# Performance work log

Hardware: AMD Instinct MI355X
Metric: run time of the kernel (lower is better)

The kernel has to match this reference:

```python
import jax, jax.numpy as jnp
import numpy as np

B, DIM, NX, NY = 4, 64, 256, 256
HEADS, DIM_HEAD, LATENT, DIM_OUT, KM = 4, 32, 128, 64, 2
DH = DIM_HEAD * KM  # LowRankKernel head dim (also RoPE dim) = 64
EPS = 1e-5
MIN_FREQ = 1.0 / 64.0  # RotaryEmbedding default in FactFormer/LNS repo


def _gelu(x):
    return jax.nn.gelu(x, approximate=False)  # torch nn.GELU default (erf)


def _conv1x1(u, w):
    # u: [b,c,h,w], w: [out,c]  (1x1 conv == channel matmul)
    return jnp.einsum('bchw,oc->bohw', u, w)


def _pooling_reducer(x, win, ln_g, ln_b, w1, w2, b2):
    # x: [b, n_keep, n_pool, c] -> Linear, mean-pool over n_pool, LN+FFN
    h = jnp.einsum('bnmc,hc->bnmh', x, win).mean(axis=2)  # [b, n, hid]
    m = h.mean(axis=-1, keepdims=True)
    v = h.var(axis=-1, keepdims=True)
    h = (h - m) / jnp.sqrt(v + EPS) * ln_g + ln_b
    return _gelu(h @ w1.T) @ w2.T + b2  # [b, n, latent]


def _rope_freqs(n):
    pos = jnp.linspace(0.0, 1.0, n) / MIN_FREQ  # scale/min_freq = 64
    inv = 1.0 / (10000.0 ** (jnp.arange(0, DH, 2, dtype=jnp.float32) / DH))
    f = pos[:, None] * inv[None, :]            # [n, DH//2]
    return jnp.concatenate([f, f], axis=-1)    # [n, DH]


def _apply_rope(x, f):
    # rotate_half = cat(-x2, x1) on half-split (FactFormer convention)
    d = x.shape[-1] // 2
    rot = jnp.concatenate([-x[..., d:], x[..., :d]], axis=-1)
    return x * jnp.cos(f) + rot * jnp.sin(f)


def _low_rank_kernel(x, wqk):
    # x: [b, n, latent] -> K: [b, heads, n, n]; scaling=1, dropout=Identity, qk_norm=False
    b, n, _ = x.shape
    qk = x @ wqk.T
    q, k = jnp.split(qk, 2, axis=-1)
    q = q.reshape(b, n, HEADS, DH).transpose(0, 2, 1, 3)
    k = k.reshape(b, n, HEADS, DH).transpose(0, 2, 1, 3)
    f = _rope_freqs(n)
    q = _apply_rope(q, f)
    k = _apply_rope(k, f)
    return jnp.einsum('bhid,bhjd->bhij', q, k)


def _forward(u, gn_w, gn_b, w_in_proj, w_to_in,
             px_win, px_ln_g, px_ln_b, px_w1, px_w2, px_b2,
             py_win, py_ln_g, py_ln_b, py_w1, py_w2, py_b2,
             kx_wqk, ky_wqk, out_w1, out_w2):
    # GroupNorm(1, dim): normalize over (C,H,W) per sample, affine
    m = u.mean(axis=(1, 2, 3), keepdims=True)
    v = u.var(axis=(1, 2, 3), keepdims=True)
    un = (u - m) / jnp.sqrt(v + EPS) * gn_w[None, :, None, None] + gn_b[None, :, None, None]
    u_phi = _conv1x1(un, w_in_proj)  # [b, heads*dim_head, nx, ny]
    ui = _conv1x1(un, w_to_in)       # [b, dim, nx, ny]
    # to_x: pool over ny -> tokens along nx; to_y: pool over nx -> tokens along ny
    ux = _pooling_reducer(ui.transpose(0, 2, 3, 1), px_win, px_ln_g, px_ln_b, px_w1, px_w2, px_b2)  # [b, nx, latent]
    uy = _pooling_reducer(ui.transpose(0, 3, 2, 1), py_win, py_ln_g, py_ln_b, py_w1, py_w2, py_b2)  # [b, ny, latent]
    kx = _low_rank_kernel(ux, kx_wqk)  # [b, h, nx, nx]
    ky = _low_rank_kernel(uy, ky_wqk)  # [b, h, ny, ny]
    b, hc, nx, ny = u_phi.shape
    up = u_phi.reshape(b, HEADS, hc // HEADS, nx, ny)
    up = jnp.einsum('bhij,bhcjm->bhcim', kx, up)
    up = jnp.einsum('bhlm,bhcim->bhcil', ky, up)
    up = up.reshape(b, hc, nx, ny)
    # InstanceNorm2d (no affine, no running stats)
    m2 = up.mean(axis=(2, 3), keepdims=True)
    v2 = up.var(axis=(2, 3), keepdims=True)
    upn = (up - m2) / jnp.sqrt(v2 + EPS)
    out = _conv1x1(_gelu(_conv1x1(upn, out_w1)), out_w2)
    return out + u


def setup_inputs() -> dict:
    key = jax.random.key(0)
    ks = jax.random.split(key, 16)
    def w(k, shape, s=0.02):
        return (jax.random.normal(k, shape) * s).astype(jnp.float32)
    return {
        'u': jax.random.normal(ks[0], (B, DIM, NX, NY), dtype=jnp.float32),
        'gn_w': jnp.ones((DIM,), jnp.float32), 'gn_b': jnp.zeros((DIM,), jnp.float32),
        'w_in_proj': w(ks[1], (HEADS * DIM_HEAD, DIM)),
        'w_to_in': w(ks[2], (DIM, DIM)),
        'px_win': w(ks[3], (DIM, DIM)),
        'px_ln_g': jnp.ones((DIM,), jnp.float32), 'px_ln_b': jnp.zeros((DIM,), jnp.float32),
        'px_w1': w(ks[4], (2 * DIM, DIM)), 'px_w2': w(ks[5], (LATENT, 2 * DIM)),
        'px_b2': jnp.zeros((LATENT,), jnp.float32),
        'py_win': w(ks[6], (DIM, DIM)),
        'py_ln_g': jnp.ones((DIM,), jnp.float32), 'py_ln_b': jnp.zeros((DIM,), jnp.float32),
        'py_w1': w(ks[7], (2 * DIM, DIM)), 'py_w2': w(ks[8], (LATENT, 2 * DIM)),
        'py_b2': jnp.zeros((LATENT,), jnp.float32),
        'kx_wqk': w(ks[9], (2 * HEADS * DH, LATENT)),
        'ky_wqk': w(ks[10], (2 * HEADS * DH, LATENT)),
        'out_w1': w(ks[11], (DIM_OUT, HEADS * DIM_HEAD)),
        'out_w2': w(ks[12], (DIM_OUT, DIM_OUT)),
    }


def reference(u, gn_w, gn_b, w_in_proj, w_to_in,
              px_win, px_ln_g, px_ln_b, px_w1, px_w2, px_b2,
              py_win, py_ln_g, py_ln_b, py_w1, py_w2, py_b2,
              kx_wqk, ky_wqk, out_w1, out_w2):
    return _forward(u, gn_w, gn_b, w_in_proj, w_to_in,
                    px_win, px_ln_g, px_ln_b, px_w1, px_w2, px_b2,
                    py_win, py_ln_g, py_ln_b, py_w1, py_w2, py_b2,
                    kx_wqk, ky_wqk, out_w1, out_w2)
```

## Files before the change

### kernel.cpp

```cpp
#include <hip/hip_runtime.h>
#include <math.h>

typedef unsigned short ushort_t;
typedef unsigned int uint_t;
typedef __attribute__((ext_vector_type(8))) short s8v;
typedef __attribute__((ext_vector_type(4))) float f4;

#define NPIX 65536
#define EPS_ 1e-5f

__device__ __forceinline__ float bf2f(ushort_t u){ return __uint_as_float(((uint_t)u)<<16); }
__device__ __forceinline__ ushort_t f2bf(float f){
  uint_t u = __float_as_uint(f);
  uint_t r = (u + 0x7fffu + ((u>>16)&1u)) >> 16;
  return (ushort_t)r;
}
__device__ __forceinline__ float bflo(uint_t p){ return __uint_as_float(p<<16); }
__device__ __forceinline__ float bfhi(uint_t p){ return __uint_as_float(p & 0xffff0000u); }
__device__ __forceinline__ uint_t packbf(float a, float b){ return (uint_t)f2bf(a) | ((uint_t)f2bf(b)<<16); }

__device__ __forceinline__ f4 MFMA(s8v a, s8v b, f4 c){
  return __builtin_amdgcn_mfma_f32_16x16x32_bf16(a, b, c, 0, 0, 0);
}

__device__ __forceinline__ float wave_sum(float v){
  #pragma unroll
  for(int m=32;m>=1;m>>=1) v += __shfl_xor(v, m, 64);
  return v;
}

__global__ __launch_bounds__(256) void k1_stats(const float* __restrict__ u,
    float* __restrict__ part, float* __restrict__ pc, float* __restrict__ poolx){
  int blk = blockIdx.x; int b = blk>>8; int c = (blk>>2)&63; int iq = blk&3;
  int t = threadIdx.x; int lane = t&63; int w = t>>6;
  const float* up = u + ((size_t)(b*64+c))*NPIX + iq*64*256;
  __shared__ float red[8];
  float cs=0.f, ss=0.f;
  for(int r=0;r<64;r++){
    float v = up[r*256 + t];
    cs += v; ss += v*v;
  }
  pc[((b*64+c)*4 + iq)*256 + t] = cs;
  float a1 = wave_sum(cs), a2 = wave_sum(ss);
  if(lane==0){ red[w]=a1; red[4+w]=a2; }
  __syncthreads();
  if(t==0){
    part[((b*64+c)*4+iq)*2]   = red[0]+red[1]+red[2]+red[3];
    part[((b*64+c)*4+iq)*2+1] = red[4]+red[5]+red[6]+red[7];
  }
  int r = t>>2, ck = t&3;
  const float* rp = up + r*256 + ck*64;
  float s=0.f;
  #pragma unroll 4
  for(int j=0;j<16;j++){
    float4 v4 = *(const float4*)(rp + j*4);
    s += v4.x + v4.y + v4.z + v4.w;
  }
  s += __shfl_xor(s, 1, 64);
  s += __shfl_xor(s, 2, 64);
  if(ck==0) poolx[(b*256 + iq*64 + r)*64 + c] = s * (1.f/256.f);
}

__global__ void k2_fin(const float* __restrict__ part, float* __restrict__ gnmv){
  int t = threadIdx.x; int b = t>>6; int i = t&63;
  float S1=0.f, S2=0.f;
  #pragma unroll
  for(int q=0;q<4;q++){
    S1 += part[((b*64+i)*4+q)*2];
    S2 += part[((b*64+i)*4+q)*2+1];
  }
  S1 = wave_sum(S1); S2 = wave_sum(S2);
  if(i==0){
    const float inv = 1.f/4194304.f;
    float m = S1*inv; float v = S2*inv - m*m;
    gnmv[b*2] = m; gnmv[b*2+1] = rsqrtf(v + EPS_);
  }
}

__global__ __launch_bounds__(256) void k2b_pool(const float* __restrict__ pc,
    float* __restrict__ pooly){
  int blk = blockIdx.x; int b = blk>>6; int c = blk&63;
  int t = threadIdx.x;
  const float* p = pc + ((size_t)(b*64+c))*4*256 + t;
  float s = p[0] + p[256] + p[512] + p[768];
  pooly[(b*256+t)*64 + c] = s * (1.f/256.f);
}

__global__ __launch_bounds__(256) void k8a_fold(const float* __restrict__ gnmv,
    const float* __restrict__ gnw, const float* __restrict__ gnb,
    const float* __restrict__ w_in_proj, const float* __restrict__ out_w2,
    ushort_t* __restrict__ wpb, float* __restrict__ c0g, ushort_t* __restrict__ w2b){
  int b = blockIdx.x; int t = threadIdx.x;
  __shared__ float scs[64], shs[64];
  if(t<64){
    float mean = gnmv[b*2], rstd = gnmv[b*2+1];
    float sc = rstd*gnw[t];
    scs[t] = sc; shs[t] = gnb[t] - mean*sc;
  }
  __syncthreads();
  int oc = t>>1, h = t&1;
  float c0 = 0.f;
  for(int k=0;k<32;k++){
    int ch = h*32 + k;
    float wv = w_in_proj[oc*64 + ch];
    wpb[((size_t)b*128 + oc)*64 + ch] = f2bf(wv*scs[ch]);
    c0 += wv*shs[ch];
  }
  c0 += __shfl_xor(c0, 1, 64);
  if(h==0) c0g[b*128 + oc] = c0;
  if(b==0){
    for(int e=t;e<4096;e+=256) w2b[e] = f2bf(out_w2[e]);
  }
}

__global__ void k8b_fold(const float* __restrict__ istat,
    const float* __restrict__ out_w1, ushort_t* __restrict__ W1b,
    float* __restrict__ bias1){
  int b = blockIdx.x; int t = threadIdx.x;
  __shared__ float ms[128], rss[128];
  ms[t] = istat[(b*128+t)*2];       rss[t] = istat[(b*128+t)*2+1];
  ms[64+t] = istat[(b*128+64+t)*2]; rss[64+t] = istat[(b*128+64+t)*2+1];
  __syncthreads();
  float bias = 0.f;
  for(int ch=0;ch<128;ch++){
    float wv = out_w1[t*128 + ch];
    float wr = wv*rss[ch];
    W1b[((size_t)b*64 + t)*128 + ch] = f2bf(wr);
    bias += wr*ms[ch];
  }
  bias1[b*64 + t] = bias;
}

__global__ __launch_bounds__(128) void k3_reduce(
    const float* __restrict__ poolx, const float* __restrict__ pooly,
    const float* __restrict__ gnmv,
    const float* __restrict__ gnw, const float* __restrict__ gnb,
    const float* __restrict__ w_to_in,
    const float* __restrict__ xwin, const float* __restrict__ xlg, const float* __restrict__ xlb,
    const float* __restrict__ xw1, const float* __restrict__ xw2, const float* __restrict__ xb2,
    const float* __restrict__ ywin, const float* __restrict__ ylg, const float* __restrict__ ylb,
    const float* __restrict__ yw1, const float* __restrict__ yw2, const float* __restrict__ yb2,
    float* __restrict__ ux, float* __restrict__ uy){
  int id = blockIdx.x;
  int side = id >> 10; int r = id & 1023; int b = r>>8; int i = r&255;
  const float* pool = side ? pooly : poolx;
  const float* win = side ? ywin : xwin;
  const float* lg  = side ? ylg  : xlg;
  const float* lb  = side ? ylb  : xlb;
  const float* w1  = side ? yw1  : xw1;
  const float* w2  = side ? yw2  : xw2;
  const float* b2  = side ? yb2  : xb2;
  float* outp = side ? uy : ux;
  int t = threadIdx.x;
  __shared__ float pn[64], t1[64], hh[64], f1[128];
  float mean = gnmv[b*2], rstd = gnmv[b*2+1];
  if(t<64){
    float pv = pool[(b*256+i)*64 + t];
    pn[t] = (pv - mean)*rstd*gnw[t] + gnb[t];
  }
  __syncthreads();
  if(t<64){
    float acc=0.f; const float* wr = w_to_in + t*64;
    #pragma unroll 8
    for(int c=0;c<64;c++) acc += pn[c]*wr[c];
    t1[t]=acc;
  }
  __syncthreads();
  if(t<64){
    float acc=0.f; const float* wr = win + t*64;
    #pragma unroll 8
    for(int c=0;c<64;c++) acc += t1[c]*wr[c];
    hh[t]=acc;
  }
  __syncthreads();
  if(t<64){
    float v = hh[t];
    float s = wave_sum(v);
    float ss = wave_sum(v*v);
    float m2 = s*(1.f/64.f);
    float var = ss*(1.f/64.f) - m2*m2;
    float rs2 = rsqrtf(var + EPS_);
    hh[t] = (v - m2)*rs2*lg[t] + lb[t];
  }
  __syncthreads();
  {
    float acc=0.f; const float* wr = w1 + t*64;
    #pragma unroll 8
    for(int c=0;c<64;c++) acc += hh[c]*wr[c];
    f1[t] = 0.5f*acc*(1.f + erff(acc*0.70710678118654752f));
  }
  __syncthreads();
  {
    float acc=0.f; const float* wr = w2 + t*128;
    #pragma unroll 8
    for(int j=0;j<128;j++) acc += f1[j]*wr[j];
    outp[(b*256+i)*128 + t] = acc + b2[t];
  }
}

__global__ __launch_bounds__(256) void k4_gemm(
    const float* __restrict__ ux, const float* __restrict__ uy,
    const float* __restrict__ wqkx, const float* __restrict__ wqky,
    ushort_t* __restrict__ qxb, ushort_t* __restrict__ kxTb,
    ushort_t* __restrict__ qyb, ushort_t* __restrict__ kyTb){
  int blk = blockIdx.x;
  int nt = blk&3; int mt = (blk>>2)&1; int b = (blk>>3)&3; int side = blk>>5;
  const float* x  = (side? uy:ux) + (size_t)(b*256 + mt*128)*128;
  const float* wq = (side? wqky:wqkx) + (size_t)nt*128*128;
  ushort_t* qb  = side? qyb : qxb;
  ushort_t* kTb = side? kyTb : kxTb;

  __shared__ __align__(16) ushort_t sA[128*136];
  __shared__ __align__(16) ushort_t sB[128*136];

  int t = threadIdx.x; int lane = t&63; int w = t>>6; int lr = lane&15; int lg = lane>>4;
  for(int e=t;e<4096;e+=256){
    int row = e>>5, c4 = (e&31)*4;
    float4 v = *(const float4*)(x + row*128 + c4);
    uint2 pk; pk.x = packbf(v.x,v.y); pk.y = packbf(v.z,v.w);
    *(uint2*)&sA[row*136 + c4] = pk;
    float4 wv = *(const float4*)(wq + row*128 + c4);
    uint2 wk; wk.x = packbf(wv.x,wv.y); wk.y = packbf(wv.z,wv.w);
    *(uint2*)&sB[row*136 + c4] = wk;
  }
  __syncthreads();
  const f4 fz = {0.f,0.f,0.f,0.f};
  f4 acc[2][8];
  #pragma unroll
  for(int it=0;it<2;it++)
    #pragma unroll
    for(int n2=0;n2<8;n2++) acc[it][n2]=fz;
  #pragma unroll
  for(int kc=0;kc<4;kc++){
    s8v bf[8];
    #pragma unroll
    for(int n2=0;n2<8;n2++)
      bf[n2] = *(const s8v*)&sB[(n2*16+lr)*136 + kc*32 + lg*8];
    #pragma unroll
    for(int it=0;it<2;it++){
      s8v a = *(const s8v*)&sA[(w*32+it*16+lr)*136 + kc*32 + lg*8];
      #pragma unroll
      for(int n2=0;n2<8;n2++)
        acc[it][n2] = MFMA(a, bf[n2], acc[it][n2]);
    }
  }
  if(nt < 2){
    #pragma unroll
    for(int it=0;it<2;it++){
      #pragma unroll
      for(int n2=0;n2<8;n2++){
        int o = nt*128 + n2*16 + lr;
        int h = o>>6, dd = o&63, t32 = dd&31;
        float invf = expf(-(float)t32*(9.210340371976184f/32.f));
        size_t base = (size_t)(b*4+h)*16384;
        #pragma unroll
        for(int r=0;r<4;r++){
          int i = mt*128 + w*32 + it*16 + lg*4 + r;
          float f = (64.f/255.f)*(float)i*invf;
          float sn, cs; __sincosf(f, &sn, &cs);
          float pair = acc[it][n2^2][r];
          float rot = ((n2&2)==0)? -pair : pair;
          float v = acc[it][n2][r]*cs + rot*sn;
          qb[base + (size_t)i*64 + dd] = f2bf(v);
        }
      }
    }
  } else {
    __syncthreads();
    #pragma unroll
    for(int it=0;it<2;it++){
      #pragma unroll
      for(int n2=0;n2<8;n2++){
        int ol = n2*16 + lr;
        int o = nt*128 + ol;
        int t32 = o&31;
        float invf = expf(-(float)t32*(9.210340371976184f/32.f));
        #pragma unroll
        for(int r=0;r<4;r++){
          int il = w*32 + it*16 + lg*4 + r;
          int i = mt*128 + il;
          float f = (64.f/255.f)*(float)i*invf;
          float sn, cs; __sincosf(f, &sn, &cs);
          float pair = acc[it][n2^2][r];
          float rot = ((n2&2)==0)? -pair : pair;
          float v = acc[it][n2][r]*cs + rot*sn;
          sA[ol*136 + il] = f2bf(v);
        }
      }
    }
    __syncthreads();
    {
      int row = t>>1, half = t&1;
      int h = (nt-2)*2 + (row>>6), dd = row&63;
      ushort_t* dst = kTb + (size_t)(b*4+h)*16384 + (size_t)dd*256 + mt*128 + half*64;
      const ushort_t* src = &sA[row*136 + half*64];
      #pragma unroll
      for(int j=0;j<8;j++)
        *(uint4*)(dst + j*8) = *(const uint4*)(src + j*8);
    }
  }
}

__global__ __launch_bounds__(256) void k5s_sums(const ushort_t* __restrict__ kxTb,
    const ushort_t* __restrict__ kyTb, float* __restrict__ ksum){
  int bh = blockIdx.x; int t = threadIdx.x;
  int row = t>>2, g = t&3;
  const ushort_t* kx = kxTb + (size_t)bh*16384 + row*256 + g*64;
  float s = 0.f;
  #pragma unroll
  for(int j=0;j<8;j++){
    uint4 v = *(const uint4*)(kx + j*8);
    s += bflo(v.x)+bfhi(v.x)+bflo(v.y)+bfhi(v.y)+bflo(v.z)+bfhi(v.z)+bflo(v.w)+bfhi(v.w);
  }
  s += __shfl_xor(s,1,64); s += __shfl_xor(s,2,64);
  if(g==0) ksum[bh*128 + row] = s;
  const ushort_t* ky = kyTb + (size_t)bh*16384 + row*256 + g*64;
  float s2 = 0.f;
  #pragma unroll
  for(int j=0;j<8;j++){
    uint4 v = *(const uint4*)(ky + j*8);
    s2 += bflo(v.x)+bfhi(v.x)+bflo(v.y)+bfhi(v.y)+bflo(v.z)+bfhi(v.z)+bflo(v.w)+bfhi(v.w);
  }
  s2 += __shfl_xor(s2,1,64); s2 += __shfl_xor(s2,2,64);
  if(g==0) ksum[bh*128 + 64 + row] = s2;
}

__global__ __launch_bounds__(512) void k7a_core(
    const float* __restrict__ u,
    const ushort_t* __restrict__ kxTb, const ushort_t* __restrict__ kyTb,
    ushort_t* __restrict__ Cb){
  int blk = blockIdx.x; int b = blk>>6;
  const float* up = u + (size_t)blk*NPIX;
  __shared__ __align__(16) ushort_t su[2][64*264];
  __shared__ __align__(16) ushort_t sT1[4][64*68];
  int t = threadIdx.x; int w = t>>6; int lane = t&63; int lr = lane&15; int lg = lane>>4;
  int h = w>>1, sub = w&1;
  const ushort_t* KyT = kyTb + (size_t)(b*4+h)*16384;
  const ushort_t* KxT = kxTb + (size_t)(b*4+h)*16384;
  const f4 fz = {0.f,0.f,0.f,0.f};
  f4 cacc[2][4];
  #pragma unroll
  for(int it=0;it<2;it++)
    #pragma unroll
    for(int et=0;et<4;et++) cacc[it][et]=fz;

  auto stageld = [&](int jc, int buf){
    #pragma unroll
    for(int k=0;k<8;k++){
      int flat = k*512 + t;
      int row = flat>>6, col4 = flat&63;
      float4 v = *(const float4*)(up + (size_t)(jc*64+row)*256 + col4*4);
      uint2 pk; pk.x = packbf(v.x,v.y); pk.y = packbf(v.z,v.w);
      *(uint2*)&su[buf][row*264 + col4*4] = pk;
    }
  };
  stageld(0, 0);
  __syncthreads();
  for(int jc=0;jc<4;jc++){
    int cur = jc&1;
    f4 acc[2][4];
    #pragma unroll
    for(int jt=0;jt<2;jt++)
      #pragma unroll
      for(int et=0;et<4;et++) acc[jt][et]=fz;
    #pragma unroll
    for(int km=0;km<8;km++){
      s8v a0 = *(const s8v*)&su[cur][(sub*32+lr)*264 + km*32 + lg*8];
      s8v a1 = *(const s8v*)&su[cur][(sub*32+16+lr)*264 + km*32 + lg*8];
      #pragma unroll
      for(int et=0;et<4;et++){
        s8v bv = *(const s8v*)(KyT + (et*16+lr)*256 + km*32 + lg*8);
        acc[0][et] = MFMA(a0,bv,acc[0][et]);
        acc[1][et] = MFMA(a1,bv,acc[1][et]);
      }
    }
    #pragma unroll
    for(int jt=0;jt<2;jt++)
      #pragma unroll
      for(int et=0;et<4;et++){
        f4 v = acc[jt][et];
        uint2 pk; pk.x=packbf(v.x,v.y); pk.y=packbf(v.z,v.w);
        *(uint2*)&sT1[h][(et*16+lr)*68 + sub*32 + jt*16 + lg*4] = pk;
      }
    __syncthreads();
    if(jc<3) stageld(jc+1, cur^1);
    #pragma unroll
    for(int kj=0;kj<2;kj++){
      s8v a0 = *(const s8v*)(KxT + (size_t)(sub*32+lr)*256 + jc*64 + kj*32 + lg*8);
      s8v a1 = *(const s8v*)(KxT + (size_t)(sub*32+16+lr)*256 + jc*64 + kj*32 + lg*8);
      #pragma unroll
      for(int et=0;et<4;et++){
        s8v bv = *(const s8v*)&sT1[h][(et*16+lr)*68 + kj*32 + lg*8];
        cacc[0][et] = MFMA(a0,bv,cacc[0][et]);
        cacc[1][et] = MFMA(a1,bv,cacc[1][et]);
      }
    }
    __syncthreads();
  }
  ushort_t* cbase = Cb + ((size_t)blk*4 + h)*4096;
  #pragma unroll
  for(int it=0;it<2;it++)
    #pragma unroll
    for(int et=0;et<4;et++){
      f4 v = cacc[it][et];
      uint2 pk; pk.x=packbf(v.x,v.y); pk.y=packbf(v.z,v.w);
      *(uint2*)&cbase[(et*16+lr)*64 + sub*32 + it*16 + lg*4] = pk;
    }
}

__global__ __launch_bounds__(256) void k7b_heavy(
    const ushort_t* __restrict__ Cb, const ushort_t* __restrict__ wpb,
    const float* __restrict__ c0g, const float* __restrict__ ksum,
    const ushort_t* __restrict__ qxb, const ushort_t* __restrict__ qyb,
    ushort_t* __restrict__ up2, float* __restrict__ istat){
  int blk = blockIdx.x;
  int c = blk & 31; int h = (blk>>5)&3; int b = blk>>7;
  int bh = b*4 + h; int ch = h*32 + c;
  const ushort_t* Qx  = qxb + (size_t)bh*16384;
  const ushort_t* Qy  = qyb + (size_t)bh*16384;
  ushort_t* out_c = up2 + (size_t)(b*128 + ch)*NPIX;

  __shared__ __align__(16) ushort_t sCT[64*72];
  __shared__ __align__(16) ushort_t sP[256*72];
  __shared__ float sW[64], sKx[64], sKy[64];
  __shared__ float sRed[8];

  int t = threadIdx.x; int w = t>>6; int lane = t&63; int lr = lane&15; int lg = lane>>4;
  if(t<64){
    sW[t]  = bf2f(wpb[((size_t)b*128 + ch)*64 + t]);
    sKx[t] = ksum[bh*128 + t];
    sKy[t] = ksum[bh*128 + 64 + t];
  }
  __syncthreads();
  {
    int e = t>>2, d0 = (t&3)*16;
    float c0 = c0g[b*128 + ch];
    float kyv = sKy[e];
    float acc[16];
    #pragma unroll
    for(int k=0;k<16;k++) acc[k] = c0*kyv*sKx[d0+k];
    const ushort_t* cbp = Cb + ((size_t)(b*64)*4 + h)*4096 + e*64 + d0;
    for(int ic=0;ic<64;ic++){
      float wv = sW[ic];
      uint4 v0 = *(const uint4*)(cbp);
      uint4 v1 = *(const uint4*)(cbp + 8);
      cbp += 16384;
      uint_t vs[8] = {v0.x,v0.y,v0.z,v0.w,v1.x,v1.y,v1.z,v1.w};
      #pragma unroll
      for(int k=0;k<8;k++){
        acc[2*k]   += wv*bflo(vs[k]);
        acc[2*k+1] += wv*bfhi(vs[k]);
      }
    }
    #pragma unroll
    for(int k=0;k<8;k++)
      *(uint_t*)&sCT[e*72 + d0 + 2*k] = packbf(acc[2*k], acc[2*k+1]);
  }
  __syncthreads();
  const f4 fz = {0.f,0.f,0.f,0.f};
  {
    s8v aF[4][2];
    #pragma unroll
    for(int me=0;me<4;me++)
      #pragma unroll
      for(int kd=0;kd<2;kd++)
        aF[me][kd] = *(const s8v*)&sCT[(me*16+lr)*72 + kd*32 + lg*8];
    #pragma unroll
    for(int it=0;it<4;it++){
      s8v b0 = *(const s8v*)(Qx + (w*64+it*16+lr)*64 + lg*8);
      s8v b1 = *(const s8v*)(Qx + (w*64+it*16+lr)*64 + 32 + lg*8);
      #pragma unroll
      for(int me=0;me<4;me++){
        f4 pv = MFMA(aF[me][0], b0, fz);
        pv = MFMA(aF[me][1], b1, pv);
        uint2 pk; pk.x=packbf(pv.x,pv.y); pk.y=packbf(pv.z,pv.w);
        *(uint2*)&sP[(w*64+it*16+lr)*72 + me*16 + lg*4] = pk;
      }
    }
  }
  __syncthreads();
  float lsum=0.f, lssq=0.f;
  {
    s8v aP[4][2];
    #pragma unroll
    for(int it=0;it<4;it++)
      #pragma unroll
      for(int ke=0;ke<2;ke++)
        aP[it][ke] = *(const s8v*)&sP[(w*64+it*16+lr)*72 + ke*32 + lg*8];
    for(int lt=0;lt<4;lt++){
      s8v bq[4][2];
      #pragma unroll
      for(int nt=0;nt<4;nt++)
        #pragma unroll
        for(int ke=0;ke<2;ke++)
          bq[nt][ke] = *(const s8v*)(Qy + (lt*64+nt*16+lr)*64 + ke*32 + lg*8);
      #pragma unroll
      for(int it=0;it<4;it++){
        #pragma unroll
        for(int nt=0;nt<4;nt++){
          f4 o = MFMA(aP[it][0], bq[nt][0], fz);
          o = MFMA(aP[it][1], bq[nt][1], o);
          #pragma unroll
          for(int r=0;r<4;r++){
            float val = o[r];
            lsum += val; lssq += val*val;
            out_c[(size_t)(w*64 + it*16 + lg*4 + r)*256 + lt*64 + nt*16 + lr] = f2bf(val);
          }
        }
      }
    }
  }
  float a1 = wave_sum(lsum), a2 = wave_sum(lssq);
  if(lane==0){ sRed[w]=a1; sRed[4+w]=a2; }
  __syncthreads();
  if(t==0){
    float S = sRed[0]+sRed[1]+sRed[2]+sRed[3];
    float SS = sRed[4]+sRed[5]+sRed[6]+sRed[7];
    float m = S*(1.f/65536.f);
    float var = SS*(1.f/65536.f) - m*m;
    istat[(b*128+ch)*2] = m;
    istat[(b*128+ch)*2+1] = rsqrtf(var + EPS_);
  }
}

__global__ __launch_bounds__(256) void kf_out(
    const ushort_t* __restrict__ up2, const ushort_t* __restrict__ W1b,
    const float* __restrict__ bias1, const ushort_t* __restrict__ w2b,
    const float* __restrict__ u, float* __restrict__ out){
  int blk = blockIdx.x;
  int b = blk>>9; int pix0 = (blk&511)<<7;
  __shared__ __align__(16) unsigned char smraw[128*132*2];
  ushort_t* sX = (ushort_t*)smraw;
  ushort_t* sG = (ushort_t*)smraw;
  float* sO = (float*)smraw;
  int t = threadIdx.x; int lane = t&63; int w = t>>6; int lr = lane&15; int lg = lane>>4;
  float4 ur[8];
  {
    int oc = t>>5; int px = (t&31)*4;
    #pragma unroll
    for(int it=0;it<8;it++){
      int o = it*8 + oc;
      ur[it] = *(const float4*)(u + ((size_t)(b*64+o))*NPIX + pix0 + px);
    }
  }
  {
    int ch = t>>4; int px = (t&15)*8;
    #pragma unroll
    for(int it=0; it<8; it++){
      int c = it*16 + ch;
      uint4 v = *(const uint4*)(up2 + ((size_t)(b*128+c))*NPIX + pix0 + px);
      uint2 lo; lo.x = v.x; lo.y = v.y;
      uint2 hi; hi.x = v.z; hi.y = v.w;
      *(uint2*)&sX[c*132 + px] = lo;
      *(uint2*)&sX[c*132 + px + 4] = hi;
    }
  }
  __syncthreads();
  const ushort_t* w1p = W1b + (size_t)b*64*128;
  f4 g[2][4];
  #pragma unroll
  for(int it=0;it<2;it++)
    #pragma unroll
    for(int nt=0;nt<4;nt++){
      float bv = -bias1[b*64 + nt*16 + lr];
      f4 ci = {bv,bv,bv,bv};
      g[it][nt] = ci;
    }
  #pragma unroll
  for(int kc=0;kc<4;kc++){
    s8v bf[4];
    #pragma unroll
    for(int nt=0;nt<4;nt++)
      bf[nt] = *(const s8v*)(w1p + (nt*16+lr)*128 + kc*32 + lg*8);
    #pragma unroll
    for(int it=0;it<2;it++){
      int pix = w*32 + it*16 + lr;
      s8v a;
      #pragma unroll
      for(int j=0;j<8;j++) a[j] = (short)sX[(kc*32+lg*8+j)*132 + pix];
      #pragma unroll
      for(int nt=0;nt<4;nt++)
        g[it][nt] = MFMA(a, bf[nt], g[it][nt]);
    }
  }
  #pragma unroll
  for(int it=0;it<2;it++)
    #pragma unroll
    for(int nt=0;nt<4;nt++){
      f4 v = g[it][nt];
      #pragma unroll
      for(int r=0;r<4;r++){
        float x = v[r];
        v[r] = 0.5f*x*(1.f + erff(x*0.70710678118654752f));
      }
      g[it][nt] = v;
    }
  __syncthreads();
  #pragma unroll
  for(int it=0;it<2;it++)
    #pragma unroll
    for(int nt=0;nt<4;nt++){
      f4 v = g[it][nt];
      uint2 pk; pk.x = packbf(v.x,v.y); pk.y = packbf(v.z,v.w);
      *(uint2*)&sG[(nt*16+lr)*132 + w*32 + it*16 + lg*4] = pk;
    }
  __syncthreads();
  f4 o2[2][4];
  const f4 fz = {0.f,0.f,0.f,0.f};
  #pragma unroll
  for(int it=0;it<2;it++)
    #pragma unroll
    for(int nt=0;nt<4;nt++) o2[it][nt]=fz;
  #pragma unroll
  for(int kc=0;kc<2;kc++){
    s8v bf[4];
    #pragma unroll
    for(int nt=0;nt<4;nt++)
      bf[nt] = *(const s8v*)(w2b + (nt*16+lr)*64 + kc*32 + lg*8);
    #pragma unroll
    for(int it=0;it<2;it++){
      int pix = w*32 + it*16 + lr;
      s8v a;
      #pragma unroll
      for(int j=0;j<8;j++) a[j] = (short)sG[(kc*32+lg*8+j)*132 + pix];
      #pragma unroll
      for(int nt=0;nt<4;nt++)
        o2[it][nt] = MFMA(a, bf[nt], o2[it][nt]);
    }
  }
  __syncthreads();
  #pragma unroll
  for(int it=0;it<2;it++)
    #pragma unroll
    for(int nt=0;nt<4;nt++)
      *(f4*)&sO[(nt*16+lr)*132 + w*32 + it*16 + lg*4] = o2[it][nt];
  __syncthreads();
  {
    int oc = t>>5; int px = (t&31)*4;
    #pragma unroll
    for(int it=0;it<8;it++){
      int o = it*8 + oc;
      float4 ov = *(const float4*)&sO[o*132 + px];
      float4 rv;
      rv.x = ov.x+ur[it].x; rv.y = ov.y+ur[it].y; rv.z = ov.z+ur[it].z; rv.w = ov.w+ur[it].w;
      *(float4*)(out + ((size_t)(b*64+o))*NPIX + pix0 + px) = rv;
    }
  }
}

extern "C" void kernel_launch(void* const* d_in, const int* in_sizes, int n_in,
                              void* d_out, int out_size, void* d_ws, size_t ws_size,
                              hipStream_t stream) {
  (void)in_sizes; (void)n_in; (void)out_size; (void)ws_size;
  const float* u        = (const float*)d_in[0];
  const float* gnw      = (const float*)d_in[1];
  const float* gnb      = (const float*)d_in[2];
  const float* w_in_proj= (const float*)d_in[3];
  const float* w_to_in  = (const float*)d_in[4];
  const float* px_win   = (const float*)d_in[5];
  const float* px_ln_g  = (const float*)d_in[6];
  const float* px_ln_b  = (const float*)d_in[7];
  const float* px_w1    = (const float*)d_in[8];
  const float* px_w2    = (const float*)d_in[9];
  const float* px_b2    = (const float*)d_in[10];
  const float* py_win   = (const float*)d_in[11];
  const float* py_ln_g  = (const float*)d_in[12];
  const float* py_ln_b  = (const float*)d_in[13];
  const float* py_w1    = (const float*)d_in[14];
  const float* py_w2    = (const float*)d_in[15];
  const float* py_b2    = (const float*)d_in[16];
  const float* kx_wqk   = (const float*)d_in[17];
  const float* ky_wqk   = (const float*)d_in[18];
  const float* out_w1   = (const float*)d_in[19];
  const float* out_w2   = (const float*)d_in[20];
  float* out = (float*)d_out;

  float* fw = (float*)d_ws;
  float* part  = fw + 0;
  float* gnmv  = fw + 2048;
  float* pc    = fw + 4096;
  float* poolx = fw + 266240;
  float* pooly = fw + 331776;
  float* ux    = fw + 397312;
  float* uy    = fw + 528384;
  float* istat = fw + 659456;
  float* c0g   = fw + 660480;
  float* bias1 = fw + 660992;
  ushort_t* wpb = (ushort_t*)(fw + 661504);
  ushort_t* W1b = (ushort_t*)(fw + 677888);
  ushort_t* w2b = (ushort_t*)(fw + 694272);
  float* ksum   = fw + 696320;
  ushort_t* qxb  = (ushort_t*)(fw + 4096);
  ushort_t* kxTb = (ushort_t*)(fw + 135168);
  ushort_t* qyb  = (ushort_t*)(fw + 698368);
  ushort_t* kyTb = (ushort_t*)(fw + 829440);
  ushort_t* up2  = (ushort_t*)(fw + 960512);
  ushort_t* Cb = (ushort_t*)d_out;

  k1_stats<<<dim3(1024), dim3(256), 0, stream>>>(u, part, pc, poolx);
  k2_fin<<<dim3(1), dim3(256), 0, stream>>>(part, gnmv);
  k2b_pool<<<dim3(256), dim3(256), 0, stream>>>(pc, pooly);
  k8a_fold<<<dim3(4), dim3(256), 0, stream>>>(gnmv, gnw, gnb, w_in_proj, out_w2, wpb, c0g, w2b);
  k3_reduce<<<dim3(2048), dim3(128), 0, stream>>>(poolx, pooly, gnmv, gnw, gnb, w_to_in,
      px_win, px_ln_g, px_ln_b, px_w1, px_w2, px_b2,
      py_win, py_ln_g, py_ln_b, py_w1, py_w2, py_b2, ux, uy);
  k4_gemm<<<dim3(64), dim3(256), 0, stream>>>(ux, uy, kx_wqk, ky_wqk, qxb, kxTb, qyb, kyTb);
  k5s_sums<<<dim3(16), dim3(256), 0, stream>>>(kxTb, kyTb, ksum);
  k7a_core<<<dim3(256), dim3(512), 0, stream>>>(u, kxTb, kyTb, Cb);
  k7b_heavy<<<dim3(512), dim3(256), 0, stream>>>(Cb, wpb, c0g, ksum, qxb, qyb, up2, istat);
  k8b_fold<<<dim3(4), dim3(64), 0, stream>>>(istat, out_w1, W1b, bias1);
  kf_out<<<dim3(2048), dim3(256), 0, stream>>>(up2, W1b, bias1, w2b, u, out);
}
```

Baseline: 222.0 us.

## Split channel-mix out of heavy kernel and halve output kernel tile

Moves the per-channel mixing of the core matrices (weighted sum over 64 input channels) out of k7b_heavy into a separate k7m_mix kernel. The new kernel stages each core tile once in shared memory and reuses it across 32 output channels, where before every heavy block re-read all 64 input-channel cores from global memory. The mixed result goes to a scratch area inside the output buffer. Separately, kf_out now handles 64 pixels per block instead of 128, doubling the grid and cutting shared memory and register use. This costs an extra kernel launch and a global round trip for the mixed matrices.

```diff
diff --git a/kernel.cpp b/kernel.cpp
--- a/kernel.cpp
+++ b/kernel.cpp
@@ -408,9 +408,67 @@
     }
 }
 
-__global__ __launch_bounds__(256) void k7b_heavy(
+__global__ __launch_bounds__(256) void k7m_mix(
     const ushort_t* __restrict__ Cb, const ushort_t* __restrict__ wpb,
     const float* __restrict__ c0g, const float* __restrict__ ksum,
+    ushort_t* __restrict__ cT){
+  int blk = blockIdx.x; int bh = blk>>4; int et = blk&15;
+  int b = bh>>2, h = bh&3;
+  __shared__ __align__(16) ushort_t sC[64*264];
+  __shared__ float sWf[32*64];
+  __shared__ float sKx[64], sKy4[4];
+  int t = threadIdx.x;
+  #pragma unroll
+  for(int k=0;k<8;k++){
+    int flat = k*256 + t;
+    int ic = flat>>5, q = flat&31;
+    uint4 v = *(const uint4*)(Cb + ((size_t)(b*64+ic)*4 + h)*4096 + et*256 + q*8);
+    *(uint4*)&sC[ic*264 + q*8] = v;
+  }
+  for(int e=t;e<2048;e+=256){
+    int ch = e>>6, ic = e&63;
+    sWf[e] = bf2f(wpb[((size_t)b*128 + h*32 + ch)*64 + ic]);
+  }
+  if(t<64) sKx[t] = ksum[bh*128 + t];
+  if(t<4)  sKy4[t] = ksum[bh*128 + 64 + et*4 + t];
+  __syncthreads();
+  int chg = t>>5, edq = t&31, ed0 = edq*8;
+  float c0v[4];
+  #pragma unroll
+  for(int cc=0;cc<4;cc++) c0v[cc] = c0g[b*128 + h*32 + chg*4 + cc];
+  float acc[4][8];
+  #pragma unroll
+  for(int j=0;j<8;j++){
+    int ed = ed0 + j;
+    float r1 = sKy4[ed>>6]*sKx[ed&63];
+    #pragma unroll
+    for(int cc=0;cc<4;cc++) acc[cc][j] = c0v[cc]*r1;
+  }
+  for(int ic=0;ic<64;ic++){
+    uint4 cv = *(const uint4*)&sC[ic*264 + ed0];
+    float x[8];
+    x[0]=bflo(cv.x); x[1]=bfhi(cv.x); x[2]=bflo(cv.y); x[3]=bfhi(cv.y);
+    x[4]=bflo(cv.z); x[5]=bfhi(cv.z); x[6]=bflo(cv.w); x[7]=bfhi(cv.w);
+    #pragma unroll
+    for(int cc=0;cc<4;cc++){
+      float wv = sWf[(chg*4+cc)*64 + ic];
+      #pragma unroll
+      for(int j=0;j<8;j++) acc[cc][j] += wv*x[j];
+    }
+  }
+  #pragma unroll
+  for(int cc=0;cc<4;cc++){
+    uint2 p0, p1;
+    p0.x = packbf(acc[cc][0],acc[cc][1]); p0.y = packbf(acc[cc][2],acc[cc][3]);
+    p1.x = packbf(acc[cc][4],acc[cc][5]); p1.y = packbf(acc[cc][6],acc[cc][7]);
+    ushort_t* dst = cT + ((size_t)bh*32 + chg*4+cc)*4096 + et*256 + ed0;
+    *(uint2*)(dst) = p0;
+    *(uint2*)(dst+4) = p1;
+  }
+}
+
+__global__ __launch_bounds__(256) void k7b_heavy(
+    const ushort_t* __restrict__ cT,
     const ushort_t* __restrict__ qxb, const ushort_t* __restrict__ qyb,
     ushort_t* __restrict__ up2, float* __restrict__ istat){
   int blk = blockIdx.x;
@@ -418,45 +476,13 @@
   int bh = b*4 + h; int ch = h*32 + c;
   const ushort_t* Qx  = qxb + (size_t)bh*16384;
   const ushort_t* Qy  = qyb + (size_t)bh*16384;
+  const ushort_t* cTc = cT + (size_t)(bh*32 + c)*4096;
   ushort_t* out_c = up2 + (size_t)(b*128 + ch)*NPIX;
 
-  __shared__ __align__(16) ushort_t sCT[64*72];
   __shared__ __align__(16) ushort_t sP[256*72];
-  __shared__ float sW[64], sKx[64], sKy[64];
   __shared__ float sRed[8];
 
   int t = threadIdx.x; int w = t>>6; int lane = t&63; int lr = lane&15; int lg = lane>>4;
-  if(t<64){
-    sW[t]  = bf2f(wpb[((size_t)b*128 + ch)*64 + t]);
-    sKx[t] = ksum[bh*128 + t];
-    sKy[t] = ksum[bh*128 + 64 + t];
-  }
-  __syncthreads();
-  {
-    int e = t>>2, d0 = (t&3)*16;
-    float c0 = c0g[b*128 + ch];
-    float kyv = sKy[e];
-    float acc[16];
-    #pragma unroll
-    for(int k=0;k<16;k++) acc[k] = c0*kyv*sKx[d0+k];
-    const ushort_t* cbp = Cb + ((size_t)(b*64)*4 + h)*4096 + e*64 + d0;
-    for(int ic=0;ic<64;ic++){
-      float wv = sW[ic];
-      uint4 v0 = *(const uint4*)(cbp);
-      uint4 v1 = *(const uint4*)(cbp + 8);
-      cbp += 16384;
-      uint_t vs[8] = {v0.x,v0.y,v0.z,v0.w,v1.x,v1.y,v1.z,v1.w};
-      #pragma unroll
-      for(int k=0;k<8;k++){
-        acc[2*k]   += wv*bflo(vs[k]);
-        acc[2*k+1] += wv*bfhi(vs[k]);
-      }
-    }
-    #pragma unroll
-    for(int k=0;k<8;k++)
-      *(uint_t*)&sCT[e*72 + d0 + 2*k] = packbf(acc[2*k], acc[2*k+1]);
-  }
-  __syncthreads();
   const f4 fz = {0.f,0.f,0.f,0.f};
   {
     s8v aF[4][2];
@@ -464,7 +490,7 @@
     for(int me=0;me<4;me++)
       #pragma unroll
       for(int kd=0;kd<2;kd++)
-        aF[me][kd] = *(const s8v*)&sCT[(me*16+lr)*72 + kd*32 + lg*8];
+        aF[me][kd] = *(const s8v*)(cTc + (me*16+lr)*64 + kd*32 + lg*8);
     #pragma unroll
     for(int it=0;it<4;it++){
       s8v b0 = *(const s8v*)(Qx + (w*64+it*16+lr)*64 + lg*8);
@@ -528,122 +554,87 @@
     const float* __restrict__ bias1, const ushort_t* __restrict__ w2b,
     const float* __restrict__ u, float* __restrict__ out){
   int blk = blockIdx.x;
-  int b = blk>>9; int pix0 = (blk&511)<<7;
-  __shared__ __align__(16) unsigned char smraw[128*132*2];
+  int b = blk>>10; int pix0 = (blk&1023)<<6;
+  __shared__ __align__(16) unsigned char smraw[128*68*2];
   ushort_t* sX = (ushort_t*)smraw;
   ushort_t* sG = (ushort_t*)smraw;
   float* sO = (float*)smraw;
   int t = threadIdx.x; int lane = t&63; int w = t>>6; int lr = lane&15; int lg = lane>>4;
-  float4 ur[8];
   {
-    int oc = t>>5; int px = (t&31)*4;
-    #pragma unroll
-    for(int it=0;it<8;it++){
-      int o = it*8 + oc;
-      ur[it] = *(const float4*)(u + ((size_t)(b*64+o))*NPIX + pix0 + px);
-    }
-  }
+    int ch = t>>1; int px = (t&1)*32;
+    #pragma unroll
+    for(int j=0;j<4;j++){
+      uint4 v = *(const uint4*)(up2 + ((size_t)(b*128+ch))*NPIX + pix0 + px + j*8);
+      *(uint4*)&sX[ch*68 + px + j*8] = v;
+    }
+  }
+  __syncthreads();
+  const ushort_t* w1p = W1b + (size_t)b*64*128;
+  f4 g[4];
+  #pragma unroll
+  for(int nt=0;nt<4;nt++){
+    float bv = -bias1[b*64 + nt*16 + lr];
+    f4 ci = {bv,bv,bv,bv};
+    g[nt] = ci;
+  }
+  #pragma unroll
+  for(int kc=0;kc<4;kc++){
+    s8v a;
+    #pragma unroll
+    for(int j=0;j<8;j++) a[j] = (short)sX[(kc*32+lg*8+j)*68 + w*16 + lr];
+    #pragma unroll
+    for(int nt=0;nt<4;nt++){
+      s8v bf = *(const s8v*)(w1p + (nt*16+lr)*128 + kc*32 + lg*8);
+      g[nt] = MFMA(a, bf, g[nt]);
+    }
+  }
+  #pragma unroll
+  for(int nt=0;nt<4;nt++){
+    f4 v = g[nt];
+    #pragma unroll
+    for(int r=0;r<4;r++){
+      float x = v[r];
+      v[r] = 0.5f*x*(1.f + erff(x*0.70710678118654752f));
+    }
+    g[nt] = v;
+  }
+  __syncthreads();
+  #pragma unroll
+  for(int nt=0;nt<4;nt++){
+    f4 v = g[nt];
+    uint2 pk; pk.x = packbf(v.x,v.y); pk.y = packbf(v.z,v.w);
+    *(uint2*)&sG[(nt*16+lr)*68 + w*16 + lg*4] = pk;
+  }
+  __syncthreads();
+  f4 o2[4];
+  const f4 fz = {0.f,0.f,0.f,0.f};
+  #pragma unroll
+  for(int nt=0;nt<4;nt++) o2[nt]=fz;
+  #pragma unroll
+  for(int kc=0;kc<2;kc++){
+    s8v a;
+    #pragma unroll
+    for(int j=0;j<8;j++) a[j] = (short)sG[(kc*32+lg*8+j)*68 + w*16 + lr];
+    #pragma unroll
+    for(int nt=0;nt<4;nt++){
+      s8v bf = *(const s8v*)(w2b + (nt*16+lr)*64 + kc*32 + lg*8);
+      o2[nt] = MFMA(a, bf, o2[nt]);
+    }
+  }
+  __syncthreads();
+  #pragma unroll
+  for(int nt=0;nt<4;nt++)
+    *(f4*)&sO[(nt*16+lr)*68 + w*16 + lg*4] = o2[nt];
+  __syncthreads();
   {
-    int ch = t>>4; int px = (t&15)*8;
-    #pragma unroll
-    for(int it=0; it<8; it++){
-      int c = it*16 + ch;
-      uint4 v = *(const uint4*)(up2 + ((size_t)(b*128+c))*NPIX + pix0 + px);
-      uint2 lo; lo.x = v.x; lo.y = v.y;
-      uint2 hi; hi.x = v.z; hi.y = v.w;
-      *(uint2*)&sX[c*132 + px] = lo;
-      *(uint2*)&sX[c*132 + px + 4] = hi;
-    }
-  }
-  __syncthreads();
-  const ushort_t* w1p = W1b + (size_t)b*64*128;
-  f4 g[2][4];
-  #pragma unroll
-  for(int it=0;it<2;it++)
-    #pragma unroll
-    for(int nt=0;nt<4;nt++){
-      float bv = -bias1[b*64 + nt*16 + lr];
-      f4 ci = {bv,bv,bv,bv};
-      g[it][nt] = ci;
-    }
-  #pragma unroll
-  for(int kc=0;kc<4;kc++){
-    s8v bf[4];
-    #pragma unroll
-    for(int nt=0;nt<4;nt++)
-      bf[nt] = *(const s8v*)(w1p + (nt*16+lr)*128 + kc*32 + lg*8);
-    #pragma unroll
-    for(int it=0;it<2;it++){
-      int pix = w*32 + it*16 + lr;
-      s8v a;
-      #pragma unroll
-      for(int j=0;j<8;j++) a[j] = (short)sX[(kc*32+lg*8+j)*132 + pix];
-      #pragma unroll
-      for(int nt=0;nt<4;nt++)
-        g[it][nt] = MFMA(a, bf[nt], g[it][nt]);
-    }
-  }
-  #pragma unroll
-  for(int it=0;it<2;it++)
-    #pragma unroll
-    for(int nt=0;nt<4;nt++){
-      f4 v = g[it][nt];
-      #pragma unroll
-      for(int r=0;r<4;r++){
-        float x = v[r];
-        v[r] = 0.5f*x*(1.f + erff(x*0.70710678118654752f));
-      }
-      g[it][nt] = v;
-    }
-  __syncthreads();
-  #pragma unroll
-  for(int it=0;it<2;it++)
-    #pragma unroll
-    for(int nt=0;nt<4;nt++){
-      f4 v = g[it][nt];
-      uint2 pk; pk.x = packbf(v.x,v.y); pk.y = packbf(v.z,v.w);
-      *(uint2*)&sG[(nt*16+lr)*132 + w*32 + it*16 + lg*4] = pk;
-    }
-  __syncthreads();
-  f4 o2[2][4];
-  const f4 fz = {0.f,0.f,0.f,0.f};
-  #pragma unroll
-  for(int it=0;it<2;it++)
-    #pragma unroll
-    for(int nt=0;nt<4;nt++) o2[it][nt]=fz;
-  #pragma unroll
-  for(int kc=0;kc<2;kc++){
-    s8v bf[4];
-    #pragma unroll
-    for(int nt=0;nt<4;nt++)
-      bf[nt] = *(const s8v*)(w2b + (nt*16+lr)*64 + kc*32 + lg*8);
-    #pragma unroll
-    for(int it=0;it<2;it++){
-      int pix = w*32 + it*16 + lr;
-      s8v a;
-      #pragma unroll
-      for(int j=0;j<8;j++) a[j] = (short)sG[(kc*32+lg*8+j)*132 + pix];
-      #pragma unroll
-      for(int nt=0;nt<4;nt++)
-        o2[it][nt] = MFMA(a, bf[nt], o2[it][nt]);
-    }
-  }
-  __syncthreads();
-  #pragma unroll
-  for(int it=0;it<2;it++)
-    #pragma unroll
-    for(int nt=0;nt<4;nt++)
-      *(f4*)&sO[(nt*16+lr)*132 + w*32 + it*16 + lg*4] = o2[it][nt];
-  __syncthreads();
-  {
-    int oc = t>>5; int px = (t&31)*4;
-    #pragma unroll
-    for(int it=0;it<8;it++){
-      int o = it*8 + oc;
-      float4 ov = *(const float4*)&sO[o*132 + px];
+    int oc = t>>2; int pxq = (t&3)*16;
+    #pragma unroll
+    for(int j=0;j<4;j++){
+      float4 ov = *(const float4*)&sO[oc*68 + pxq + j*4];
+      float4 uv = *(const float4*)(u + ((size_t)(b*64+oc))*NPIX + pix0 + pxq + j*4);
       float4 rv;
-      rv.x = ov.x+ur[it].x; rv.y = ov.y+ur[it].y; rv.z = ov.z+ur[it].z; rv.w = ov.w+ur[it].w;
-      *(float4*)(out + ((size_t)(b*64+o))*NPIX + pix0 + px) = rv;
+      rv.x = ov.x+uv.x; rv.y = ov.y+uv.y; rv.z = ov.z+uv.z; rv.w = ov.w+uv.w;
+      *(float4*)(out + ((size_t)(b*64+oc))*NPIX + pix0 + pxq + j*4) = rv;
     }
   }
 }
@@ -696,6 +687,7 @@
   ushort_t* kyTb = (ushort_t*)(fw + 829440);
   ushort_t* up2  = (ushort_t*)(fw + 960512);
   ushort_t* Cb = (ushort_t*)d_out;
+  ushort_t* cT = (ushort_t*)d_out + 4194304;
 
   k1_stats<<<dim3(1024), dim3(256), 0, stream>>>(u, part, pc, poolx);
   k2_fin<<<dim3(1), dim3(256), 0, stream>>>(part, gnmv);
@@ -707,7 +699,8 @@
   k4_gemm<<<dim3(64), dim3(256), 0, stream>>>(ux, uy, kx_wqk, ky_wqk, qxb, kxTb, qyb, kyTb);
   k5s_sums<<<dim3(16), dim3(256), 0, stream>>>(kxTb, kyTb, ksum);
   k7a_core<<<dim3(256), dim3(512), 0, stream>>>(u, kxTb, kyTb, Cb);
-  k7b_heavy<<<dim3(512), dim3(256), 0, stream>>>(Cb, wpb, c0g, ksum, qxb, qyb, up2, istat);
+  k7m_mix<<<dim3(256), dim3(256), 0, stream>>>(Cb, wpb, c0g, ksum, cT);
+  k7b_heavy<<<dim3(512), dim3(256), 0, stream>>>(cT, qxb, qyb, up2, istat);
   k8b_fold<<<dim3(4), dim3(64), 0, stream>>>(istat, out_w1, W1b, bias1);
-  kf_out<<<dim3(2048), dim3(256), 0, stream>>>(up2, W1b, bias1, w2b, u, out);
-}
+  kf_out<<<dim3(4096), dim3(256), 0, stream>>>(up2, W1b, bias1, w2b, u, out);
+}
```

Result: slower. 227.6 us (+2.5%).

## Split channel-mix into separate kernel, vectorize heavy stores, defer residual loads

Applied to the files above, without the earlier changes.

Moves the per-channel mixing of the core tensor out of k7b_heavy into a new k7m_mix kernel that stages a tile of Cb in shared memory and computes four output channels per thread group, so each Cb element is reused across channels instead of being re-read from global memory by every channel block. k7b_heavy now reads the precomputed mixed tensor directly as MFMA operands. It also swaps the MFMA operand order so each lane writes four contiguous bf16 outputs as one packed store instead of four scattered scalar stores. kf_out loads the residual input just before it is added rather than holding it in registers across the GEMMs, which lowers register pressure. The cost is an extra kernel launch and an intermediate buffer round trip through memory placed inside the output allocation.

```diff
diff --git a/kernel.cpp b/kernel.cpp
--- a/kernel.cpp
+++ b/kernel.cpp
@@ -408,9 +408,67 @@
     }
 }
 
-__global__ __launch_bounds__(256) void k7b_heavy(
+__global__ __launch_bounds__(256) void k7m_mix(
     const ushort_t* __restrict__ Cb, const ushort_t* __restrict__ wpb,
     const float* __restrict__ c0g, const float* __restrict__ ksum,
+    ushort_t* __restrict__ cT){
+  int blk = blockIdx.x; int bh = blk>>4; int et = blk&15;
+  int b = bh>>2, h = bh&3;
+  __shared__ __align__(16) ushort_t sC[64*264];
+  __shared__ float sWf[32*64];
+  __shared__ float sKx[64], sKy4[4];
+  int t = threadIdx.x;
+  #pragma unroll
+  for(int k=0;k<8;k++){
+    int flat = k*256 + t;
+    int ic = flat>>5, q = flat&31;
+    uint4 v = *(const uint4*)(Cb + ((size_t)(b*64+ic)*4 + h)*4096 + et*256 + q*8);
+    *(uint4*)&sC[ic*264 + q*8] = v;
+  }
+  for(int e=t;e<2048;e+=256){
+    int ch = e>>6, ic = e&63;
+    sWf[e] = bf2f(wpb[((size_t)b*128 + h*32 + ch)*64 + ic]);
+  }
+  if(t<64) sKx[t] = ksum[bh*128 + t];
+  if(t<4)  sKy4[t] = ksum[bh*128 + 64 + et*4 + t];
+  __syncthreads();
+  int chg = t>>5, edq = t&31, ed0 = edq*8;
+  float c0v[4];
+  #pragma unroll
+  for(int cc=0;cc<4;cc++) c0v[cc] = c0g[b*128 + h*32 + chg*4 + cc];
+  float acc[4][8];
+  #pragma unroll
+  for(int j=0;j<8;j++){
+    int ed = ed0 + j;
+    float r1 = sKy4[ed>>6]*sKx[ed&63];
+    #pragma unroll
+    for(int cc=0;cc<4;cc++) acc[cc][j] = c0v[cc]*r1;
+  }
+  for(int ic=0;ic<64;ic++){
+    uint4 cv = *(const uint4*)&sC[ic*264 + ed0];
+    float x[8];
+    x[0]=bflo(cv.x); x[1]=bfhi(cv.x); x[2]=bflo(cv.y); x[3]=bfhi(cv.y);
+    x[4]=bflo(cv.z); x[5]=bfhi(cv.z); x[6]=bflo(cv.w); x[7]=bfhi(cv.w);
+    #pragma unroll
+    for(int cc=0;cc<4;cc++){
+      float wv = sWf[(chg*4+cc)*64 + ic];
+      #pragma unroll
+      for(int j=0;j<8;j++) acc[cc][j] += wv*x[j];
+    }
+  }
+  #pragma unroll
+  for(int cc=0;cc<4;cc++){
+    uint2 p0, p1;
+    p0.x = packbf(acc[cc][0],acc[cc][1]); p0.y = packbf(acc[cc][2],acc[cc][3]);
+    p1.x = packbf(acc[cc][4],acc[cc][5]); p1.y = packbf(acc[cc][6],acc[cc][7]);
+    ushort_t* dst = cT + ((size_t)bh*32 + chg*4+cc)*4096 + et*256 + ed0;
+    *(uint2*)(dst) = p0;
+    *(uint2*)(dst+4) = p1;
+  }
+}
+
+__global__ __launch_bounds__(256) void k7b_heavy(
+    const ushort_t* __restrict__ cT,
     const ushort_t* __restrict__ qxb, const ushort_t* __restrict__ qyb,
     ushort_t* __restrict__ up2, float* __restrict__ istat){
   int blk = blockIdx.x;
@@ -418,45 +476,13 @@
   int bh = b*4 + h; int ch = h*32 + c;
   const ushort_t* Qx  = qxb + (size_t)bh*16384;
   const ushort_t* Qy  = qyb + (size_t)bh*16384;
+  const ushort_t* cTc = cT + (size_t)(bh*32 + c)*4096;
   ushort_t* out_c = up2 + (size_t)(b*128 + ch)*NPIX;
 
-  __shared__ __align__(16) ushort_t sCT[64*72];
   __shared__ __align__(16) ushort_t sP[256*72];
-  __shared__ float sW[64], sKx[64], sKy[64];
   __shared__ float sRed[8];
 
   int t = threadIdx.x; int w = t>>6; int lane = t&63; int lr = lane&15; int lg = lane>>4;
-  if(t<64){
-    sW[t]  = bf2f(wpb[((size_t)b*128 + ch)*64 + t]);
-    sKx[t] = ksum[bh*128 + t];
-    sKy[t] = ksum[bh*128 + 64 + t];
-  }
-  __syncthreads();
-  {
-    int e = t>>2, d0 = (t&3)*16;
-    float c0 = c0g[b*128 + ch];
-    float kyv = sKy[e];
-    float acc[16];
-    #pragma unroll
-    for(int k=0;k<16;k++) acc[k] = c0*kyv*sKx[d0+k];
-    const ushort_t* cbp = Cb + ((size_t)(b*64)*4 + h)*4096 + e*64 + d0;
-    for(int ic=0;ic<64;ic++){
-      float wv = sW[ic];
-      uint4 v0 = *(const uint4*)(cbp);
-      uint4 v1 = *(const uint4*)(cbp + 8);
-      cbp += 16384;
-      uint_t vs[8] = {v0.x,v0.y,v0.z,v0.w,v1.x,v1.y,v1.z,v1.w};
-      #pragma unroll
-      for(int k=0;k<8;k++){
-        acc[2*k]   += wv*bflo(vs[k]);
-        acc[2*k+1] += wv*bfhi(vs[k]);
-      }
-    }
-    #pragma unroll
-    for(int k=0;k<8;k++)
-      *(uint_t*)&sCT[e*72 + d0 + 2*k] = packbf(acc[2*k], acc[2*k+1]);
-  }
-  __syncthreads();
   const f4 fz = {0.f,0.f,0.f,0.f};
   {
     s8v aF[4][2];
@@ -464,7 +490,7 @@
     for(int me=0;me<4;me++)
       #pragma unroll
       for(int kd=0;kd<2;kd++)
-        aF[me][kd] = *(const s8v*)&sCT[(me*16+lr)*72 + kd*32 + lg*8];
+        aF[me][kd] = *(const s8v*)(cTc + (me*16+lr)*64 + kd*32 + lg*8);
     #pragma unroll
     for(int it=0;it<4;it++){
       s8v b0 = *(const s8v*)(Qx + (w*64+it*16+lr)*64 + lg*8);
@@ -498,14 +524,12 @@
       for(int it=0;it<4;it++){
         #pragma unroll
         for(int nt=0;nt<4;nt++){
-          f4 o = MFMA(aP[it][0], bq[nt][0], fz);
-          o = MFMA(aP[it][1], bq[nt][1], o);
-          #pragma unroll
-          for(int r=0;r<4;r++){
-            float val = o[r];
-            lsum += val; lssq += val*val;
-            out_c[(size_t)(w*64 + it*16 + lg*4 + r)*256 + lt*64 + nt*16 + lr] = f2bf(val);
-          }
+          f4 o = MFMA(bq[nt][0], aP[it][0], fz);
+          o = MFMA(bq[nt][1], aP[it][1], o);
+          lsum += o[0]+o[1]+o[2]+o[3];
+          lssq += o[0]*o[0]+o[1]*o[1]+o[2]*o[2]+o[3]*o[3];
+          uint2 pk; pk.x = packbf(o[0],o[1]); pk.y = packbf(o[2],o[3]);
+          *(uint2*)(out_c + (size_t)(w*64 + it*16 + lr)*256 + lt*64 + nt*16 + lg*4) = pk;
         }
       }
     }
@@ -534,15 +558,6 @@
   ushort_t* sG = (ushort_t*)smraw;
   float* sO = (float*)smraw;
   int t = threadIdx.x; int lane = t&63; int w = t>>6; int lr = lane&15; int lg = lane>>4;
-  float4 ur[8];
-  {
-    int oc = t>>5; int px = (t&31)*4;
-    #pragma unroll
-    for(int it=0;it<8;it++){
-      int o = it*8 + oc;
-      ur[it] = *(const float4*)(u + ((size_t)(b*64+o))*NPIX + pix0 + px);
-    }
-  }
   {
     int ch = t>>4; int px = (t&15)*8;
     #pragma unroll
@@ -641,8 +656,9 @@
     for(int it=0;it<8;it++){
       int o = it*8 + oc;
       float4 ov = *(const float4*)&sO[o*132 + px];
+      float4 uv = *(const float4*)(u + ((size_t)(b*64+o))*NPIX + pix0 + px);
       float4 rv;
-      rv.x = ov.x+ur[it].x; rv.y = ov.y+ur[it].y; rv.z = ov.z+ur[it].z; rv.w = ov.w+ur[it].w;
+      rv.x = ov.x+uv.x; rv.y = ov.y+uv.y; rv.z = ov.z+uv.z; rv.w = ov.w+uv.w;
       *(float4*)(out + ((size_t)(b*64+o))*NPIX + pix0 + px) = rv;
     }
   }
@@ -696,6 +712,7 @@
   ushort_t* kyTb = (ushort_t*)(fw + 829440);
   ushort_t* up2  = (ushort_t*)(fw + 960512);
   ushort_t* Cb = (ushort_t*)d_out;
+  ushort_t* cT = (ushort_t*)d_out + 4194304;
 
   k1_stats<<<dim3(1024), dim3(256), 0, stream>>>(u, part, pc, poolx);
   k2_fin<<<dim3(1), dim3(256), 0, stream>>>(part, gnmv);
@@ -707,7 +724,8 @@
   k4_gemm<<<dim3(64), dim3(256), 0, stream>>>(ux, uy, kx_wqk, ky_wqk, qxb, kxTb, qyb, kyTb);
   k5s_sums<<<dim3(16), dim3(256), 0, stream>>>(kxTb, kyTb, ksum);
   k7a_core<<<dim3(256), dim3(512), 0, stream>>>(u, kxTb, kyTb, Cb);
-  k7b_heavy<<<dim3(512), dim3(256), 0, stream>>>(Cb, wpb, c0g, ksum, qxb, qyb, up2, istat);
+  k7m_mix<<<dim3(256), dim3(256), 0, stream>>>(Cb, wpb, c0g, ksum, cT);
+  k7b_heavy<<<dim3(512), dim3(256), 0, stream>>>(cT, qxb, qyb, up2, istat);
   k8b_fold<<<dim3(4), dim3(64), 0, stream>>>(istat, out_w1, W1b, bias1);
   kf_out<<<dim3(2048), dim3(256), 0, stream>>>(up2, W1b, bias1, w2b, u, out);
 }
```

After: 210.5 us. -5.2%, faster.
